# Kernel optimization log

Hardware: AMD Instinct MI355X
Metric: run time of the kernel (lower is better)

## Reference

```python
import jax, jax.numpy as jnp
import numpy as np

N_ENT = 50000
N_EDGE = 500000
D = 256          # ent_hidden_size
H1, C1 = 8, 64   # conv1: heads=8, out=64, concat -> 512
NEG_SLOPE = 0.2
LN_EPS = 1e-5


def setup_inputs() -> dict:
    key = jax.random.key(0)
    ks = jax.random.split(key, 12)
    s = 0.05  # small init scale for numerical sanity
    return {
        "edge_index": jax.random.randint(ks[0], (2, N_EDGE), 0, N_ENT),
        "x": jax.random.normal(ks[1], (N_ENT, D), dtype=jnp.float32),
        "ln_w": jnp.ones((D,), jnp.float32),
        "ln_b": jnp.zeros((D,), jnp.float32),
        "W1": jax.random.normal(ks[2], (D, H1 * C1), dtype=jnp.float32) * s,
        "att_src1": jax.random.normal(ks[3], (H1, C1), dtype=jnp.float32) * s,
        "att_dst1": jax.random.normal(ks[4], (H1, C1), dtype=jnp.float32) * s,
        "b1": jnp.zeros((H1 * C1,), jnp.float32),
        "W2": jax.random.normal(ks[5], (H1 * C1, D), dtype=jnp.float32) * s,
        "att_src2": jax.random.normal(ks[6], (1, D), dtype=jnp.float32) * s,
        "att_dst2": jax.random.normal(ks[7], (1, D), dtype=jnp.float32) * s,
        "b2": jnp.zeros((D,), jnp.float32),
    }


def _gat_conv(x, edge_index, W, att_src, att_dst, bias, heads, out_ch, concat):
    """PyG GATConv (shared src/dst lin, add_self_loops=True, eval-mode dropout)."""
    n = x.shape[0]
    loops = jnp.arange(n)
    src = jnp.concatenate([edge_index[0], loops])  # [E+N]
    dst = jnp.concatenate([edge_index[1], loops])

    h = (x @ W).reshape(n, heads, out_ch)                 # [N,H,C]
    a_src = jnp.sum(h * att_src[None], axis=-1)           # [N,H]
    a_dst = jnp.sum(h * att_dst[None], axis=-1)           # [N,H]

    e = jax.nn.leaky_relu(a_src[src] + a_dst[dst], NEG_SLOPE)  # [E+N,H]
    # per-destination segment softmax (every dst has a self-loop -> no empties)
    m = jax.lax.stop_gradient(jax.ops.segment_max(e, dst, num_segments=n))
    p = jnp.exp(e - m[dst])
    denom = jax.ops.segment_sum(p, dst, num_segments=n)
    alpha = p / denom[dst]                                # [E+N,H]

    out = jax.ops.segment_sum(h[src] * alpha[..., None], dst, num_segments=n)  # [N,H,C]
    out = out.reshape(n, heads * out_ch) if concat else out.mean(axis=1)
    return out + bias


def reference(edge_index, x, ln_w, ln_b, W1, att_src1, att_dst1, b1,
              W2, att_src2, att_dst2, b2):
    # LayerNorm(ent_hidden), eps=1e-5; dropouts are eval-mode no-ops
    mu = jnp.mean(x, axis=-1, keepdims=True)
    var = jnp.var(x, axis=-1, keepdims=True)
    h = (x - mu) / jnp.sqrt(var + LN_EPS) * ln_w + ln_b
    h = jax.nn.elu(_gat_conv(h, edge_index, W1, att_src1, att_dst1, b1, H1, C1, True))
    return _gat_conv(h, edge_index, W2, att_src2, att_dst2, b2, 1, D, False)
```

## Files before the change

### kernel.cpp

```cpp
#include <hip/hip_runtime.h>
#include <hip/hip_bf16.h>
#include <cstdint>

#define N_ENT  50000
#define N_EDGE 500000
#define D_IN   256
constexpr int ETOT = N_EDGE + N_ENT;

typedef __attribute__((ext_vector_type(8))) short bfrag;
typedef __attribute__((ext_vector_type(4))) float f4acc;
typedef __attribute__((ext_vector_type(4))) float f32x4;
typedef __attribute__((ext_vector_type(8))) short s16x8;

__device__ __forceinline__ float lrelu(float x) { return x > 0.f ? x : 0.2f * x; }
__device__ __forceinline__ float eluf(float x)  { return x > 0.f ? x : (expf(x) - 1.f); }
__device__ __forceinline__ short to_bf16(float f) {
    __hip_bfloat16 b = __float2bfloat16(f);
    return *(short*)&b;
}
__device__ __forceinline__ float2 bf2_to_f32(unsigned int u) {
    float2 r;
    r.x = __uint_as_float(u << 16);
    r.y = __uint_as_float(u & 0xffff0000u);
    return r;
}

__global__ __launch_bounds__(256) void ln_kernel(const float* __restrict__ x,
        const float* __restrict__ w, const float* __restrict__ b,
        short* __restrict__ y)
{
    int n = blockIdx.x * 4 + (threadIdx.x >> 6);
    int lane = threadIdx.x & 63;
    const f32x4 v = __builtin_nontemporal_load((const f32x4*)(x + (size_t)n * D_IN + lane * 4));
    float s  = v.x + v.y + v.z + v.w;
    float sq = v.x*v.x + v.y*v.y + v.z*v.z + v.w*v.w;
    #pragma unroll
    for (int off = 1; off < 64; off <<= 1) {
        s  += __shfl_xor(s, off);
        sq += __shfl_xor(sq, off);
    }
    float mean = s * (1.f / 256.f);
    float var  = sq * (1.f / 256.f) - mean * mean;
    float rstd = rsqrtf(var + 1e-5f);
    float4 wv = *(const float4*)(w + lane * 4);
    float4 bv = *(const float4*)(b + lane * 4);
    short4 o;
    o.x = to_bf16((v.x - mean) * rstd * wv.x + bv.x);
    o.y = to_bf16((v.y - mean) * rstd * wv.y + bv.y);
    o.z = to_bf16((v.z - mean) * rstd * wv.z + bv.z);
    o.w = to_bf16((v.w - mean) * rstd * wv.w + bv.w);
    *(short4*)(y + (size_t)n * D_IN + lane * 4) = o;
}

__global__ __launch_bounds__(256) void transpose_bf16_kernel(const float* __restrict__ W,
        short* __restrict__ WT, int R, int C)
{
    int i = blockIdx.x * 256 + threadIdx.x;
    if (i >= R * C) return;
    int r = i / C, c = i - r * C;
    WT[c * R + r] = to_bf16(W[i]);
}

template<int NN, int KK>
__global__ __launch_bounds__(256) void gemm_mfma(const short* __restrict__ A,
        const short* __restrict__ BT, short* __restrict__ C, int M)
{
    __shared__ short As[128 * 32];
    __shared__ short Bs[128 * 32];
    const int tid  = threadIdx.x;
    const int w    = tid >> 6;
    const int l    = tid & 63;
    const int wm   = w >> 1, wn = w & 1;
    const int m0   = blockIdx.y * 128;
    const int n0   = blockIdx.x * 128;
    const int quad = l >> 4;
    const int ln16 = l & 15;
    const int rl   = l >> 2;
    const int cs   = l & 3;

    f4acc acc[4][4];
    #pragma unroll
    for (int i = 0; i < 4; ++i)
        #pragma unroll
        for (int j = 0; j < 4; ++j)
            acc[i][j] = (f4acc){0.f, 0.f, 0.f, 0.f};

    for (int k0 = 0; k0 < KK; k0 += 32) {
        __syncthreads();
        #pragma unroll
        for (int tt = 0; tt < 2; ++tt) {
            int t   = w * 2 + tt;
            int row = t * 16 + rl;
            int ca  = cs ^ ((row >> 1) & 3);
            const short* ga = A + (size_t)(m0 + row) * KK + k0 + ca * 8;
            __builtin_amdgcn_global_load_lds(
                (const __attribute__((address_space(1))) unsigned int*)ga,
                (__attribute__((address_space(3))) unsigned int*)&As[t * 512], 16, 0, 0);
            const short* gb = BT + (size_t)(n0 + row) * KK + k0 + ca * 8;
            __builtin_amdgcn_global_load_lds(
                (const __attribute__((address_space(1))) unsigned int*)gb,
                (__attribute__((address_space(3))) unsigned int*)&Bs[t * 512], 16, 0, 0);
        }
        __syncthreads();
        bfrag af[4], bf[4];
        #pragma unroll
        for (int i = 0; i < 4; ++i) {
            int r = wm * 64 + i * 16 + ln16;
            af[i] = *(const bfrag*)&As[r * 32 + (quad ^ ((r >> 1) & 3)) * 8];
            int rn = wn * 64 + i * 16 + ln16;
            bf[i] = *(const bfrag*)&Bs[rn * 32 + (quad ^ ((rn >> 1) & 3)) * 8];
        }
        #pragma unroll
        for (int i = 0; i < 4; ++i)
            #pragma unroll
            for (int j = 0; j < 4; ++j)
                acc[i][j] = __builtin_amdgcn_mfma_f32_16x16x32_bf16(af[i], bf[j], acc[i][j], 0, 0, 0);
    }
    #pragma unroll
    for (int i = 0; i < 4; ++i) {
        #pragma unroll
        for (int p = 0; p < 4; ++p) {
            int gr = m0 + wm * 64 + i * 16 + quad * 4 + p;
            if (gr < M) {
                #pragma unroll
                for (int j = 0; j < 4; ++j) {
                    int gc = n0 + wn * 64 + j * 16 + ln16;
                    C[(size_t)gr * NN + gc] = to_bf16(acc[i][j][p]);
                }
            }
        }
    }
}

template<int H, int C>
__global__ __launch_bounds__(256) void attn_dots_kernel(const short* __restrict__ feat,
        const float* __restrict__ att_s, const float* __restrict__ att_d,
        float* __restrict__ a_s, float* __restrict__ a_d, int N)
{
    constexpr int F = H * C;
    constexpr int PL = F / 64;
    int n = blockIdx.x * 4 + (threadIdx.x >> 6);
    if (n >= N) return;
    int lane = threadIdx.x & 63;
    int f0 = lane * PL;
    int h = f0 / C;
    float fv[PL];
    const unsigned int* fp = (const unsigned int*)(feat + (size_t)n * F + f0);
    #pragma unroll
    for (int j = 0; j < PL / 2; ++j) {
        float2 t = bf2_to_f32(fp[j]);
        fv[2 * j] = t.x; fv[2 * j + 1] = t.y;
    }
    float ps = 0.f, pd = 0.f;
    #pragma unroll
    for (int j = 0; j < PL; ++j) {
        ps = fmaf(fv[j], att_s[f0 + j], ps);
        pd = fmaf(fv[j], att_d[f0 + j], pd);
    }
    constexpr int GROUP = 64 / H;
    #pragma unroll
    for (int off = 1; off < GROUP; off <<= 1) {
        ps += __shfl_xor(ps, off);
        pd += __shfl_xor(pd, off);
    }
    if ((lane & (GROUP - 1)) == 0) {
        a_s[(size_t)n * H + h] = ps;
        a_d[(size_t)n * H + h] = pd;
    }
}

__global__ __launch_bounds__(256) void count_kernel(const int* __restrict__ ei,
        int* __restrict__ cnt)
{
    int e = blockIdx.x * 256 + threadIdx.x;
    if (e < N_EDGE) atomicAdd(&cnt[ei[N_EDGE + e]], 1);
}

__global__ __launch_bounds__(256) void alloc_kernel(const int* __restrict__ cnt,
        int* __restrict__ row_start, int* __restrict__ cursor)
{
    int d = blockIdx.x * 256 + threadIdx.x;
    int lane = threadIdx.x & 63;
    int c = (d < N_ENT) ? cnt[d] : 0;
    int inc = c;
    #pragma unroll
    for (int off = 1; off < 64; off <<= 1) {
        int nb = __shfl_up(inc, off);
        if (lane >= off) inc += nb;
    }
    int waveTotal = __shfl(inc, 63);
    int base = 0;
    if (lane == 63) base = atomicAdd(cursor, waveTotal);
    base = __shfl(base, 63);
    if (d < N_ENT) row_start[d] = base + inc - c;
}

__global__ __launch_bounds__(256) void fill_csr_kernel(const int* __restrict__ ei,
        const int* __restrict__ row_start, int* __restrict__ cursor2,
        int* __restrict__ csr_src)
{
    int e = blockIdx.x * 256 + threadIdx.x;
    if (e >= N_EDGE) return;
    int d = ei[N_EDGE + e];
    int pos = atomicAdd(&cursor2[d], 1);
    csr_src[row_start[d] + pos] = ei[e];
}

__global__ __launch_bounds__(256) void aggr1_kernel(const int* __restrict__ csr_src,
        const int* __restrict__ row_start, const int* __restrict__ cnt,
        const short* __restrict__ feat, const float* __restrict__ a_s,
        const float* __restrict__ a_d, const float* __restrict__ bias,
        short* __restrict__ out)
{
    int d = blockIdx.x * 4 + (threadIdx.x >> 6);
    if (d >= N_ENT) return;
    int lane = threadIdx.x & 63;
    int f0 = lane * 8;
    int h = lane >> 3;
    int rs = row_start[d];
    int n = cnt[d];
    float adh = a_d[d * 8 + h];

    float den = 0.f;
    float acc[8] = {0.f, 0.f, 0.f, 0.f, 0.f, 0.f, 0.f, 0.f};
    {
        float p = __expf(lrelu(a_s[d * 8 + h] + adh));
        den += p;
        uint4 rv = *(const uint4*)(feat + (size_t)d * 512 + f0);
        float2 t0 = bf2_to_f32(rv.x), t1 = bf2_to_f32(rv.y);
        float2 t2 = bf2_to_f32(rv.z), t3 = bf2_to_f32(rv.w);
        acc[0] += p * t0.x; acc[1] += p * t0.y; acc[2] += p * t1.x; acc[3] += p * t1.y;
        acc[4] += p * t2.x; acc[5] += p * t2.y; acc[6] += p * t3.x; acc[7] += p * t3.y;
    }
    int i = 0;
    for (; i + 8 <= n; i += 8) {
        int   sv[8];
        float ev[8];
        uint4 rv[8];
        #pragma unroll
        for (int u = 0; u < 8; ++u) sv[u] = csr_src[rs + i + u];
        #pragma unroll
        for (int u = 0; u < 8; ++u) ev[u] = a_s[sv[u] * 8 + h];
        #pragma unroll
        for (int u = 0; u < 8; ++u) rv[u] = *(const uint4*)(feat + (size_t)sv[u] * 512 + f0);
        #pragma unroll
        for (int u = 0; u < 8; ++u) {
            float p = __expf(lrelu(ev[u] + adh));
            den += p;
            float2 t0 = bf2_to_f32(rv[u].x), t1 = bf2_to_f32(rv[u].y);
            float2 t2 = bf2_to_f32(rv[u].z), t3 = bf2_to_f32(rv[u].w);
            acc[0] += p * t0.x; acc[1] += p * t0.y; acc[2] += p * t1.x; acc[3] += p * t1.y;
            acc[4] += p * t2.x; acc[5] += p * t2.y; acc[6] += p * t3.x; acc[7] += p * t3.y;
        }
    }
    for (; i + 4 <= n; i += 4) {
        int   sv[4];
        float ev[4];
        uint4 rv[4];
        #pragma unroll
        for (int u = 0; u < 4; ++u) sv[u] = csr_src[rs + i + u];
        #pragma unroll
        for (int u = 0; u < 4; ++u) ev[u] = a_s[sv[u] * 8 + h];
        #pragma unroll
        for (int u = 0; u < 4; ++u) rv[u] = *(const uint4*)(feat + (size_t)sv[u] * 512 + f0);
        #pragma unroll
        for (int u = 0; u < 4; ++u) {
            float p = __expf(lrelu(ev[u] + adh));
            den += p;
            float2 t0 = bf2_to_f32(rv[u].x), t1 = bf2_to_f32(rv[u].y);
            float2 t2 = bf2_to_f32(rv[u].z), t3 = bf2_to_f32(rv[u].w);
            acc[0] += p * t0.x; acc[1] += p * t0.y; acc[2] += p * t1.x; acc[3] += p * t1.y;
            acc[4] += p * t2.x; acc[5] += p * t2.y; acc[6] += p * t3.x; acc[7] += p * t3.y;
        }
    }
    for (; i < n; ++i) {
        int s = csr_src[rs + i];
        float p = __expf(lrelu(a_s[s * 8 + h] + adh));
        den += p;
        uint4 rv = *(const uint4*)(feat + (size_t)s * 512 + f0);
        float2 t0 = bf2_to_f32(rv.x), t1 = bf2_to_f32(rv.y);
        float2 t2 = bf2_to_f32(rv.z), t3 = bf2_to_f32(rv.w);
        acc[0] += p * t0.x; acc[1] += p * t0.y; acc[2] += p * t1.x; acc[3] += p * t1.y;
        acc[4] += p * t2.x; acc[5] += p * t2.y; acc[6] += p * t3.x; acc[7] += p * t3.y;
    }
    float inv = 1.f / den;
    float4 b0 = *(const float4*)(bias + f0);
    float4 b1 = *(const float4*)(bias + f0 + 4);
    s16x8 o;
    o[0] = to_bf16(eluf(acc[0] * inv + b0.x)); o[1] = to_bf16(eluf(acc[1] * inv + b0.y));
    o[2] = to_bf16(eluf(acc[2] * inv + b0.z)); o[3] = to_bf16(eluf(acc[3] * inv + b0.w));
    o[4] = to_bf16(eluf(acc[4] * inv + b1.x)); o[5] = to_bf16(eluf(acc[5] * inv + b1.y));
    o[6] = to_bf16(eluf(acc[6] * inv + b1.z)); o[7] = to_bf16(eluf(acc[7] * inv + b1.w));
    __builtin_nontemporal_store(o, (s16x8*)(out + (size_t)d * 512 + f0));
}

__global__ __launch_bounds__(256) void aggr2_kernel(const int* __restrict__ csr_src,
        const int* __restrict__ row_start, const int* __restrict__ cnt,
        const short* __restrict__ feat, const float* __restrict__ a_s,
        const float* __restrict__ a_d, const float* __restrict__ bias,
        float* __restrict__ out)
{
    int d = blockIdx.x * 4 + (threadIdx.x >> 6);
    if (d >= N_ENT) return;
    int lane = threadIdx.x & 63;
    int half = lane >> 5;
    int li   = lane & 31;
    int f0   = li * 8;
    int rs = row_start[d];
    int n = cnt[d];
    float adh = a_d[d];

    float den = 0.f;
    float acc[8] = {0.f, 0.f, 0.f, 0.f, 0.f, 0.f, 0.f, 0.f};
    {
        float p = (half == 0) ? __expf(lrelu(a_s[d] + adh)) : 0.f;
        uint4 rv = *(const uint4*)(feat + (size_t)d * 256 + f0);
        den += p;
        float2 t0 = bf2_to_f32(rv.x), t1 = bf2_to_f32(rv.y);
        float2 t2 = bf2_to_f32(rv.z), t3 = bf2_to_f32(rv.w);
        acc[0] += p * t0.x; acc[1] += p * t0.y; acc[2] += p * t1.x; acc[3] += p * t1.y;
        acc[4] += p * t2.x; acc[5] += p * t2.y; acc[6] += p * t3.x; acc[7] += p * t3.y;
    }
    int i = 0;
    for (; i + 4 <= n; i += 4) {
        int e0 = i + half, e1 = i + 2 + half;
        int s0 = csr_src[rs + e0];
        int s1 = csr_src[rs + e1];
        float a0 = a_s[s0], a1 = a_s[s1];
        uint4 rv0 = *(const uint4*)(feat + (size_t)s0 * 256 + f0);
        uint4 rv1 = *(const uint4*)(feat + (size_t)s1 * 256 + f0);
        float p0 = __expf(lrelu(a0 + adh));
        float p1 = __expf(lrelu(a1 + adh));
        den += p0 + p1;
        float2 t0, t1, t2, t3;
        t0 = bf2_to_f32(rv0.x); t1 = bf2_to_f32(rv0.y); t2 = bf2_to_f32(rv0.z); t3 = bf2_to_f32(rv0.w);
        acc[0] += p0 * t0.x; acc[1] += p0 * t0.y; acc[2] += p0 * t1.x; acc[3] += p0 * t1.y;
        acc[4] += p0 * t2.x; acc[5] += p0 * t2.y; acc[6] += p0 * t3.x; acc[7] += p0 * t3.y;
        t0 = bf2_to_f32(rv1.x); t1 = bf2_to_f32(rv1.y); t2 = bf2_to_f32(rv1.z); t3 = bf2_to_f32(rv1.w);
        acc[0] += p1 * t0.x; acc[1] += p1 * t0.y; acc[2] += p1 * t1.x; acc[3] += p1 * t1.y;
        acc[4] += p1 * t2.x; acc[5] += p1 * t2.y; acc[6] += p1 * t3.x; acc[7] += p1 * t3.y;
    }
    for (; i < n; i += 2) {
        int e = i + half;
        bool valid = e < n;
        int s = valid ? csr_src[rs + e] : d;
        float av = a_s[s];
        uint4 rv = *(const uint4*)(feat + (size_t)s * 256 + f0);
        float p = valid ? __expf(lrelu(av + adh)) : 0.f;
        den += p;
        float2 t0 = bf2_to_f32(rv.x), t1 = bf2_to_f32(rv.y);
        float2 t2 = bf2_to_f32(rv.z), t3 = bf2_to_f32(rv.w);
        acc[0] += p * t0.x; acc[1] += p * t0.y; acc[2] += p * t1.x; acc[3] += p * t1.y;
        acc[4] += p * t2.x; acc[5] += p * t2.y; acc[6] += p * t3.x; acc[7] += p * t3.y;
    }
    den += __shfl_xor(den, 32);
    #pragma unroll
    for (int k = 0; k < 8; ++k) acc[k] += __shfl_xor(acc[k], 32);

    float inv = 1.f / den;
    if (half == 0) {
        float4 b0 = *(const float4*)(bias + f0);
        float4 b1 = *(const float4*)(bias + f0 + 4);
        f32x4 o0, o1;
        o0.x = acc[0] * inv + b0.x; o0.y = acc[1] * inv + b0.y;
        o0.z = acc[2] * inv + b0.z; o0.w = acc[3] * inv + b0.w;
        o1.x = acc[4] * inv + b1.x; o1.y = acc[5] * inv + b1.y;
        o1.z = acc[6] * inv + b1.z; o1.w = acc[7] * inv + b1.w;
        __builtin_nontemporal_store(o0, (f32x4*)(out + (size_t)d * 256 + f0));
        __builtin_nontemporal_store(o1, (f32x4*)(out + (size_t)d * 256 + f0 + 4));
    }
}

extern "C" void kernel_launch(void* const* d_in, const int* in_sizes, int n_in,
                              void* d_out, int out_size, void* d_ws, size_t ws_size,
                              hipStream_t stream)
{
    const int*   ei     = (const int*)  d_in[0];
    const float* x      = (const float*)d_in[1];
    const float* ln_w   = (const float*)d_in[2];
    const float* ln_b   = (const float*)d_in[3];
    const float* W1     = (const float*)d_in[4];
    const float* att_s1 = (const float*)d_in[5];
    const float* att_d1 = (const float*)d_in[6];
    const float* b1     = (const float*)d_in[7];
    const float* W2     = (const float*)d_in[8];
    const float* att_s2 = (const float*)d_in[9];
    const float* att_d2 = (const float*)d_in[10];
    const float* b2     = (const float*)d_in[11];
    float* out = (float*)d_out;

    short* h0b = (short*)d_ws;
    short* h1b = h0b + 12800000;
    short* h2b = h1b + 25600000;
    short* h3b = h2b + 25600000;
    short* W1T = h3b + 12800000;
    short* W2T = W1T + 131072;
    float* a_s1 = (float*)(W2T + 131072);
    float* a_d1 = a_s1 + 400000;
    float* a_s2 = a_d1 + 400000;
    float* a_d2 = a_s2 + 50000;
    int* cnt       = (int*)(a_d2 + 50000);
    int* row_start = cnt + 50000;
    int* cursor2   = row_start + 50000;
    int* csr_src   = cursor2 + 50000;
    int* cursor    = csr_src + 500000;

    hipMemsetAsync(cnt,     0, 50000 * 4, stream);
    hipMemsetAsync(cursor2, 0, 50000 * 4, stream);
    hipMemsetAsync(cursor,  0, 4, stream);

    count_kernel<<<(N_EDGE + 255) / 256, 256, 0, stream>>>(ei, cnt);
    alloc_kernel<<<(N_ENT + 255) / 256, 256, 0, stream>>>(cnt, row_start, cursor);
    fill_csr_kernel<<<(N_EDGE + 255) / 256, 256, 0, stream>>>(ei, row_start, cursor2, csr_src);

    transpose_bf16_kernel<<<(131072 + 255) / 256, 256, 0, stream>>>(W1, W1T, 256, 512);
    transpose_bf16_kernel<<<(131072 + 255) / 256, 256, 0, stream>>>(W2, W2T, 512, 256);

    ln_kernel<<<12500, 256, 0, stream>>>(x, ln_w, ln_b, h0b);

    gemm_mfma<512, 256><<<dim3(4, 391), 256, 0, stream>>>(h0b, W1T, h1b, N_ENT);
    attn_dots_kernel<8, 64><<<12500, 256, 0, stream>>>(h1b, att_s1, att_d1, a_s1, a_d1, N_ENT);
    aggr1_kernel<<<12500, 256, 0, stream>>>(csr_src, row_start, cnt, h1b, a_s1, a_d1, b1, h2b);

    gemm_mfma<256, 512><<<dim3(2, 391), 256, 0, stream>>>(h2b, W2T, h3b, N_ENT);
    attn_dots_kernel<1, 256><<<12500, 256, 0, stream>>>(h3b, att_s2, att_d2, a_s2, a_d2, N_ENT);
    aggr2_kernel<<<12500, 256, 0, stream>>>(csr_src, row_start, cnt, h3b, a_s2, a_d2, b2, out);
}
```

Before: 409.9 us.

## Fuse prep kernels and layer-1 attention dots into GEMM epilogue

Merges LayerNorm, edge-degree counting and both weight transposes into one multi-role prep kernel, and collapses three memsets into one. Computes the layer-1 per-head attention logits inside the first GEMM's epilogue from fp32 accumulators, which removes a separate pass that re-reads the 512-wide bf16 feature matrix. Also drops the 8-way unrolled gather loop in aggr1, leaving only the 4-way loop, which may lower memory-level parallelism. The fused dots now use unrounded fp32 values instead of bf16-rounded features, so results change slightly.

```diff
diff --git a/kernel.cpp b/kernel.cpp
--- a/kernel.cpp
+++ b/kernel.cpp
@@ -25,45 +25,54 @@
     return r;
 }
 
-__global__ __launch_bounds__(256) void ln_kernel(const float* __restrict__ x,
-        const float* __restrict__ w, const float* __restrict__ b,
-        short* __restrict__ y)
-{
-    int n = blockIdx.x * 4 + (threadIdx.x >> 6);
-    int lane = threadIdx.x & 63;
-    const f32x4 v = __builtin_nontemporal_load((const f32x4*)(x + (size_t)n * D_IN + lane * 4));
-    float s  = v.x + v.y + v.z + v.w;
-    float sq = v.x*v.x + v.y*v.y + v.z*v.z + v.w*v.w;
-    #pragma unroll
-    for (int off = 1; off < 64; off <<= 1) {
-        s  += __shfl_xor(s, off);
-        sq += __shfl_xor(sq, off);
-    }
-    float mean = s * (1.f / 256.f);
-    float var  = sq * (1.f / 256.f) - mean * mean;
-    float rstd = rsqrtf(var + 1e-5f);
-    float4 wv = *(const float4*)(w + lane * 4);
-    float4 bv = *(const float4*)(b + lane * 4);
-    short4 o;
-    o.x = to_bf16((v.x - mean) * rstd * wv.x + bv.x);
-    o.y = to_bf16((v.y - mean) * rstd * wv.y + bv.y);
-    o.z = to_bf16((v.z - mean) * rstd * wv.z + bv.z);
-    o.w = to_bf16((v.w - mean) * rstd * wv.w + bv.w);
-    *(short4*)(y + (size_t)n * D_IN + lane * 4) = o;
-}
-
-__global__ __launch_bounds__(256) void transpose_bf16_kernel(const float* __restrict__ W,
-        short* __restrict__ WT, int R, int C)
-{
-    int i = blockIdx.x * 256 + threadIdx.x;
-    if (i >= R * C) return;
-    int r = i / C, c = i - r * C;
-    WT[c * R + r] = to_bf16(W[i]);
-}
-
-template<int NN, int KK>
+__global__ __launch_bounds__(256) void prep_kernel(const float* __restrict__ x,
+        const float* __restrict__ lnw, const float* __restrict__ lnb,
+        short* __restrict__ y, const int* __restrict__ ei, int* __restrict__ cnt,
+        const float* __restrict__ W1, short* __restrict__ W1T,
+        const float* __restrict__ W2, short* __restrict__ W2T)
+{
+    int blk = blockIdx.x;
+    if (blk < 12500) {
+        int n = blk * 4 + (threadIdx.x >> 6);
+        int lane = threadIdx.x & 63;
+        const f32x4 v = __builtin_nontemporal_load((const f32x4*)(x + (size_t)n * D_IN + lane * 4));
+        float s  = v.x + v.y + v.z + v.w;
+        float sq = v.x*v.x + v.y*v.y + v.z*v.z + v.w*v.w;
+        #pragma unroll
+        for (int off = 1; off < 64; off <<= 1) {
+            s  += __shfl_xor(s, off);
+            sq += __shfl_xor(sq, off);
+        }
+        float mean = s * (1.f / 256.f);
+        float var  = sq * (1.f / 256.f) - mean * mean;
+        float rstd = rsqrtf(var + 1e-5f);
+        float4 wv = *(const float4*)(lnw + lane * 4);
+        float4 bv = *(const float4*)(lnb + lane * 4);
+        short4 o;
+        o.x = to_bf16((v.x - mean) * rstd * wv.x + bv.x);
+        o.y = to_bf16((v.y - mean) * rstd * wv.y + bv.y);
+        o.z = to_bf16((v.z - mean) * rstd * wv.z + bv.z);
+        o.w = to_bf16((v.w - mean) * rstd * wv.w + bv.w);
+        *(short4*)(y + (size_t)n * D_IN + lane * 4) = o;
+    } else if (blk < 14454) {
+        int e = (blk - 12500) * 256 + threadIdx.x;
+        if (e < N_EDGE) atomicAdd(&cnt[ei[N_EDGE + e]], 1);
+    } else if (blk < 14966) {
+        int i = (blk - 14454) * 256 + threadIdx.x;
+        int r = i >> 9, c = i & 511;
+        W1T[c * 256 + r] = to_bf16(W1[i]);
+    } else {
+        int i = (blk - 14966) * 256 + threadIdx.x;
+        int r = i >> 8, c = i & 255;
+        W2T[c * 512 + r] = to_bf16(W2[i]);
+    }
+}
+
+template<int NN, int KK, bool FUSE_DOTS>
 __global__ __launch_bounds__(256) void gemm_mfma(const short* __restrict__ A,
-        const short* __restrict__ BT, short* __restrict__ C, int M)
+        const short* __restrict__ BT, short* __restrict__ C,
+        const float* __restrict__ att_s, const float* __restrict__ att_d,
+        float* __restrict__ a_s, float* __restrict__ a_d, int M)
 {
     __shared__ short As[128 * 32];
     __shared__ short Bs[128 * 32];
@@ -116,16 +125,48 @@
             for (int j = 0; j < 4; ++j)
                 acc[i][j] = __builtin_amdgcn_mfma_f32_16x16x32_bf16(af[i], bf[j], acc[i][j], 0, 0, 0);
     }
+
+    float as_c[4], ad_c[4];
+    if constexpr (FUSE_DOTS) {
+        #pragma unroll
+        for (int j = 0; j < 4; ++j) {
+            int gc = n0 + wn * 64 + j * 16 + ln16;
+            as_c[j] = att_s[gc];
+            ad_c[j] = att_d[gc];
+        }
+    }
+    const int hh = (n0 + wn * 64) >> 6;
+
     #pragma unroll
     for (int i = 0; i < 4; ++i) {
         #pragma unroll
         for (int p = 0; p < 4; ++p) {
             int gr = m0 + wm * 64 + i * 16 + quad * 4 + p;
+            float ps = 0.f, pd = 0.f;
+            if constexpr (FUSE_DOTS) {
+                #pragma unroll
+                for (int j = 0; j < 4; ++j) {
+                    float c = acc[i][j][p];
+                    ps = fmaf(c, as_c[j], ps);
+                    pd = fmaf(c, ad_c[j], pd);
+                }
+                #pragma unroll
+                for (int off = 1; off < 16; off <<= 1) {
+                    ps += __shfl_xor(ps, off);
+                    pd += __shfl_xor(pd, off);
+                }
+            }
             if (gr < M) {
                 #pragma unroll
                 for (int j = 0; j < 4; ++j) {
                     int gc = n0 + wn * 64 + j * 16 + ln16;
                     C[(size_t)gr * NN + gc] = to_bf16(acc[i][j][p]);
+                }
+                if constexpr (FUSE_DOTS) {
+                    if (ln16 == 0) {
+                        a_s[(size_t)gr * (NN / 64) + hh] = ps;
+                        a_d[(size_t)gr * (NN / 64) + hh] = pd;
+                    }
                 }
             }
         }
@@ -167,13 +208,6 @@
         a_s[(size_t)n * H + h] = ps;
         a_d[(size_t)n * H + h] = pd;
     }
-}
-
-__global__ __launch_bounds__(256) void count_kernel(const int* __restrict__ ei,
-        int* __restrict__ cnt)
-{
-    int e = blockIdx.x * 256 + threadIdx.x;
-    if (e < N_EDGE) atomicAdd(&cnt[ei[N_EDGE + e]], 1);
 }
 
 __global__ __launch_bounds__(256) void alloc_kernel(const int* __restrict__ cnt,
@@ -233,26 +267,6 @@
         acc[4] += p * t2.x; acc[5] += p * t2.y; acc[6] += p * t3.x; acc[7] += p * t3.y;
     }
     int i = 0;
-    for (; i + 8 <= n; i += 8) {
-        int   sv[8];
-        float ev[8];
-        uint4 rv[8];
-        #pragma unroll
-        for (int u = 0; u < 8; ++u) sv[u] = csr_src[rs + i + u];
-        #pragma unroll
-        for (int u = 0; u < 8; ++u) ev[u] = a_s[sv[u] * 8 + h];
-        #pragma unroll
-        for (int u = 0; u < 8; ++u) rv[u] = *(const uint4*)(feat + (size_t)sv[u] * 512 + f0);
-        #pragma unroll
-        for (int u = 0; u < 8; ++u) {
-            float p = __expf(lrelu(ev[u] + adh));
-            den += p;
-            float2 t0 = bf2_to_f32(rv[u].x), t1 = bf2_to_f32(rv[u].y);
-            float2 t2 = bf2_to_f32(rv[u].z), t3 = bf2_to_f32(rv[u].w);
-            acc[0] += p * t0.x; acc[1] += p * t0.y; acc[2] += p * t1.x; acc[3] += p * t1.y;
-            acc[4] += p * t2.x; acc[5] += p * t2.y; acc[6] += p * t3.x; acc[7] += p * t3.y;
-        }
-    }
     for (; i + 4 <= n; i += 4) {
         int   sv[4];
         float ev[4];
@@ -400,29 +414,23 @@
     float* a_s2 = a_d1 + 400000;
     float* a_d2 = a_s2 + 50000;
     int* cnt       = (int*)(a_d2 + 50000);
-    int* row_start = cnt + 50000;
-    int* cursor2   = row_start + 50000;
-    int* csr_src   = cursor2 + 50000;
-    int* cursor    = csr_src + 500000;
-
-    hipMemsetAsync(cnt,     0, 50000 * 4, stream);
-    hipMemsetAsync(cursor2, 0, 50000 * 4, stream);
-    hipMemsetAsync(cursor,  0, 4, stream);
-
-    count_kernel<<<(N_EDGE + 255) / 256, 256, 0, stream>>>(ei, cnt);
-    alloc_kernel<<<(N_ENT + 255) / 256, 256, 0, stream>>>(cnt, row_start, cursor);
-    fill_csr_kernel<<<(N_EDGE + 255) / 256, 256, 0, stream>>>(ei, row_start, cursor2, csr_src);
-
-    transpose_bf16_kernel<<<(131072 + 255) / 256, 256, 0, stream>>>(W1, W1T, 256, 512);
-    transpose_bf16_kernel<<<(131072 + 255) / 256, 256, 0, stream>>>(W2, W2T, 512, 256);
-
-    ln_kernel<<<12500, 256, 0, stream>>>(x, ln_w, ln_b, h0b);
-
-    gemm_mfma<512, 256><<<dim3(4, 391), 256, 0, stream>>>(h0b, W1T, h1b, N_ENT);
-    attn_dots_kernel<8, 64><<<12500, 256, 0, stream>>>(h1b, att_s1, att_d1, a_s1, a_d1, N_ENT);
+    int* cursor2   = cnt + 50000;
+    int* cursor    = cursor2 + 50000;
+    int* row_start = cursor + 1;
+    int* csr_src   = row_start + 50000;
+
+    hipMemsetAsync(cnt, 0, 100001 * 4, stream);
+
+    prep_kernel<<<15478, 256, 0, stream>>>(x, ln_w, ln_b, h0b, ei, cnt, W1, W1T, W2, W2T);
+    alloc_kernel<<<196, 256, 0, stream>>>(cnt, row_start, cursor);
+    fill_csr_kernel<<<1954, 256, 0, stream>>>(ei, row_start, cursor2, csr_src);
+
+    gemm_mfma<512, 256, true><<<dim3(4, 391), 256, 0, stream>>>(
+        h0b, W1T, h1b, att_s1, att_d1, a_s1, a_d1, N_ENT);
     aggr1_kernel<<<12500, 256, 0, stream>>>(csr_src, row_start, cnt, h1b, a_s1, a_d1, b1, h2b);
 
-    gemm_mfma<256, 512><<<dim3(2, 391), 256, 0, stream>>>(h2b, W2T, h3b, N_ENT);
+    gemm_mfma<256, 512, false><<<dim3(2, 391), 256, 0, stream>>>(
+        h2b, W2T, h3b, nullptr, nullptr, nullptr, nullptr, N_ENT);
     attn_dots_kernel<1, 256><<<12500, 256, 0, stream>>>(h3b, att_s2, att_d2, a_s2, a_d2, N_ENT);
     aggr2_kernel<<<12500, 256, 0, stream>>>(csr_src, row_start, cnt, h3b, a_s2, a_d2, b2, out);
 }
```

Result: no change. 403.9 us (-1.5%).
